# Performance work log

Measured on AMD Instinct MI355X. Metric: run time of the kernel, lower is better.

Reference implementation:

```python
import jax, jax.numpy as jnp
import numpy as np

B, D = 4096, 1024
TEMPERATURE = 0.07


def setup_inputs() -> dict:
    key = jax.random.key(0)
    k1, k2, k3, k4, k5, k6 = jax.random.split(key, 6)
    return {
        "mri_features": jax.random.normal(k1, (B, D), dtype=jnp.float32),
        "pet_features": jax.random.normal(k2, (B, D), dtype=jnp.float32),
        "labels": jax.random.randint(k3, (B,), 0, 3, dtype=jnp.int64),
        "subtype_mri": jax.random.randint(k4, (B,), 0, 4, dtype=jnp.int64),
        "subtype_pet": jax.random.randint(k5, (B,), 0, 4, dtype=jnp.int64),
        "clinical_similarity": jax.random.uniform(k6, (B, B), dtype=jnp.float32),
    }


def _build_weights(labels, subtype_mri, subtype_pet, clinical_similarity):
    # vectorized form of the O(B^2) python loop
    same_label = labels[:, None] == labels[None, :]
    label_zero = labels[:, None] == 0
    sub_match = (subtype_mri[:, None] == subtype_mri[None, :]) & (
        subtype_pet[:, None] == subtype_pet[None, :]
    )
    n = labels.shape[0]
    not_diag = ~jnp.eye(n, dtype=bool)
    mask = same_label & (label_zero | sub_match) & not_diag
    weights = jnp.where(mask, clinical_similarity, 0.0)
    row_sums = weights.sum(axis=1, keepdims=True)
    row_sums = jnp.where(row_sums == 0, 1.0, row_sums)
    return weights / row_sums


def _contrastive(fi, fj, weights):
    fi = fi / jnp.linalg.norm(fi, axis=1, keepdims=True)
    fj = fj / jnp.linalg.norm(fj, axis=1, keepdims=True)
    sim = jnp.matmul(fi, fj.T) / TEMPERATURE  # [B, B]
    log_sm = jax.nn.log_softmax(sim, axis=1)
    return -jnp.sum(weights * log_sm) / fi.shape[0]


def reference(mri_features, pet_features, labels, subtype_mri, subtype_pet, clinical_similarity):
    weights = _build_weights(labels, subtype_mri, subtype_pet, clinical_similarity)
    pairs = [
        (mri_features, pet_features),
        (pet_features, mri_features),
        (mri_features, mri_features),
        (pet_features, pet_features),
    ]
    total = 0.0
    for fi, fj in pairs:
        total = total + _contrastive(fi, fj, weights)
    return total / len(pairs)
```

## Files before the change

### kernel.cpp

```cpp
#include <hip/hip_runtime.h>
#include <hip/hip_bf16.h>
#include <hip/hip_fp8.h>
#include <math.h>

typedef __attribute__((ext_vector_type(4))) float f32x4;

#define NB 4096
#define ND 1024
#define INV_T 14.2857142857142857f

__device__ inline float fp82f(unsigned char b) {
    __hip_fp8_e4m3 h; h.__x = b;
    return (float)h;
}
__device__ inline void gload16(const void* g, void* l) {
    __builtin_amdgcn_global_load_lds(
        (const __attribute__((address_space(1))) void*)g,
        (__attribute__((address_space(3))) void*)l, 16, 0, 0);
}

__global__ __launch_bounds__(256) void norm_kernel(
        const float* __restrict__ M, const float* __restrict__ P,
        unsigned char* __restrict__ Mf, unsigned char* __restrict__ Pf) {
    int row = blockIdx.x & (NB - 1);
    const float* src = (blockIdx.x < NB) ? M : P;
    unsigned char* dst = (blockIdx.x < NB) ? Mf : Pf;
    int tid = threadIdx.x;
    float4 v = ((const float4*)(src + (size_t)row * ND))[tid];
    float ss = v.x * v.x + v.y * v.y + v.z * v.z + v.w * v.w;
    for (int off = 32; off; off >>= 1) ss += __shfl_down(ss, off);
    __shared__ float red[4];
    int lane = tid & 63, w = tid >> 6;
    if (lane == 0) red[w] = ss;
    __syncthreads();
    float rn = rsqrtf(red[0] + red[1] + red[2] + red[3]);
    int p = __builtin_amdgcn_cvt_pk_fp8_f32(v.x * rn, v.y * rn, 0, false);
    p = __builtin_amdgcn_cvt_pk_fp8_f32(v.z * rn, v.w * rn, p, true);
    ((int*)dst)[row * 256 + tid] = p;
}

__global__ __launch_bounds__(256) void key_kernel(
        const int* __restrict__ labels, const int* __restrict__ sm,
        const int* __restrict__ sp, int* __restrict__ code) {
    int i = blockIdx.x * 256 + threadIdx.x;
    if (i < NB) {
        int l = labels[i];
        code[i] = (l == 0) ? 0x40000000 : (1 + l + (sm[i] << 8) + (sp[i] << 16));
    }
}

__global__ __launch_bounds__(256) void rowsumw_kernel(
        const float* __restrict__ cs, const int* __restrict__ code,
        unsigned char* __restrict__ W, float* __restrict__ flag) {
    int i = blockIdx.x;
    int ci = code[i];
    int tid = threadIdx.x;
    const float4* row = (const float4*)(cs + (size_t)i * NB);
    const int4* c4 = (const int4*)code;
    float4 v[4];
    int4 cj[4];
    float s = 0.f;
#pragma unroll
    for (int k = 0; k < 4; ++k) {
        int t = tid + k * 256;
        v[k] = row[t];
        cj[k] = c4[t];
        int j = t * 4;
        if (cj[k].x == ci && j + 0 != i) s += v[k].x;
        if (cj[k].y == ci && j + 1 != i) s += v[k].y;
        if (cj[k].z == ci && j + 2 != i) s += v[k].z;
        if (cj[k].w == ci && j + 3 != i) s += v[k].w;
    }
    for (int off = 1; off < 64; off <<= 1) s += __shfl_xor(s, off);
    __shared__ float red[4];
    int lane = tid & 63, w = tid >> 6;
    if (lane == 0) red[w] = s;
    __syncthreads();
    float tot = red[0] + red[1] + red[2] + red[3];
    float inv = (tot > 0.f) ? 1.f / tot : 0.f;
#pragma unroll
    for (int k = 0; k < 4; ++k) {
        int t = tid + k * 256;
        int j = t * 4;
        float f0 = (cj[k].x == ci && j + 0 != i) ? v[k].x * inv : 0.f;
        float f1 = (cj[k].y == ci && j + 1 != i) ? v[k].y * inv : 0.f;
        float f2 = (cj[k].z == ci && j + 2 != i) ? v[k].z * inv : 0.f;
        float f3 = (cj[k].w == ci && j + 3 != i) ? v[k].w * inv : 0.f;
        int p = __builtin_amdgcn_cvt_pk_fp8_f32(f0, f1, 0, false);
        p = __builtin_amdgcn_cvt_pk_fp8_f32(f2, f3, p, true);
        ((int*)W)[((size_t)i * NB + j) >> 2] = p;
    }
    if (tid == 0) flag[i] = (tot > 0.f) ? 1.f : 0.f;
}

__global__ __launch_bounds__(256, 3) void mega_gemm(
        const unsigned char* __restrict__ Mf, const unsigned char* __restrict__ Pf,
        const unsigned char* __restrict__ Wg,
        float* __restrict__ outs) {
    __shared__ char smem[49152] __attribute__((aligned(16)));

    int tid = threadIdx.x;
    int lane = tid & 63, w = tid >> 6;
    int wm = w >> 1, wn = w & 1;
    int lr = lane & 15, lg = lane >> 4;

    int b = (blockIdx.x & 7) * 260 + (blockIdx.x >> 3);
    int bi, bj, mode;
    const unsigned char *A, *Bm;
    if (b < 1024) {
        int st = b >> 4;
        int sb = b & 15;
        bi = (st >> 3) * 4 + (sb >> 2);
        bj = (st & 7) * 4 + (sb & 3);
        A = Mf; Bm = Pf; mode = 0;
    } else {
        int s = b - 1024;
        int md = (s >= 528) ? 1 : 0;
        s -= md * 528;
        bi = 0;
        while (s >= 32 - bi) { s -= 32 - bi; ++bi; }
        bj = bi + s;
        A = md ? Pf : Mf; Bm = A;
        mode = 1 + md;
    }
    bool offdiag = (bi != bj);
    size_t rowBase = (size_t)bi * 128;
    size_t colBase = (size_t)bj * 128;
    bool needW2 = (rowBase != colBase);
    float* rowTgt = outs + ((mode == 0) ? 0 : (mode == 1) ? 8192 : 12288);
    float* colTgt = (mode == 0) ? (outs + 4096) : rowTgt;

    int sr = lane >> 2;
    int scs = (lane & 3) ^ (sr & 3) ^ ((sr >> 2) & 3);
    const unsigned char* gA = A + (rowBase + w * 32 + sr) * ND + scs * 16;
    const unsigned char* gB = Bm + (colBase + w * 32 + sr) * ND + scs * 16;

    f32x4 acc[4][4] = {};

#define STAGE(bufi, t) {                                                    \
        int k0_ = (t) * 64;                                                 \
        char* baseA_ = smem + (bufi) * 16384;                               \
        char* baseB_ = baseA_ + 8192;                                       \
        gload16(gA + k0_,                   baseA_ + (w * 2    ) * 1024);   \
        gload16(gA + (size_t)16 * ND + k0_, baseA_ + (w * 2 + 1) * 1024);   \
        gload16(gB + k0_,                   baseB_ + (w * 2    ) * 1024);   \
        gload16(gB + (size_t)16 * ND + k0_, baseB_ + (w * 2 + 1) * 1024);   \
    }
#define STAGEW(dst, rbase, cbase) {                                         \
        _Pragma("unroll")                                                   \
        for (int c = 0; c < 4; ++c) {                                       \
            int q_ = w * 4 + c;                                             \
            int sw_ = 8 * q_ + (lane >> 3);                                 \
            int gch_ = (lane & 7) ^ (sw_ & 7);                              \
            gload16(Wg + ((rbase) + sw_) * (size_t)NB + (cbase) + gch_ * 16,\
                    (dst) + q_ * 1024);                                     \
        }                                                                   \
    }
#define COMPUTE(bufi) {                                                     \
        const unsigned char* sA = (const unsigned char*)(smem + (bufi) * 16384); \
        const unsigned char* sB = sA + 8192;                                \
        int rx = (lr & 3) ^ ((lr >> 2) & 3);                                \
        _Pragma("unroll 1")                                                 \
        for (int ks = 0; ks < 2; ++ks) {                                    \
            int cp = (((ks * 2) + (lg >> 1)) ^ rx) * 16 + (lg & 1) * 8;     \
            long av[4], bv[4];                                              \
            _Pragma("unroll")                                               \
            for (int n = 0; n < 4; ++n)                                     \
                bv[n] = *(const long*)&sB[(wn * 64 + n * 16 + lr) * 64 + cp]; \
            _Pragma("unroll")                                               \
            for (int i = 0; i < 4; ++i)                                     \
                av[i] = *(const long*)&sA[(wm * 64 + i * 16 + lr) * 64 + cp]; \
            _Pragma("unroll")                                               \
            for (int i = 0; i < 4; ++i)                                     \
                _Pragma("unroll")                                           \
                for (int n = 0; n < 4; ++n)                                 \
                    acc[i][n] = __builtin_amdgcn_mfma_f32_16x16x32_fp8_fp8( \
                        av[i], bv[n], acc[i][n], 0, 0, 0);                  \
        }                                                                   \
    }
#define BAR __builtin_amdgcn_s_barrier()

    STAGE(0, 0); STAGE(1, 1);
    asm volatile("s_waitcnt vmcnt(4)" ::: "memory"); BAR;
    for (int t = 0; t < 14; ++t) {
        STAGE((t + 2) % 3, t + 2);
        COMPUTE(t % 3);
        asm volatile("s_waitcnt vmcnt(4)" ::: "memory"); BAR;
    }
    STAGEW(smem + 16384, rowBase, colBase);
    COMPUTE(2);
    BAR;
    if (needW2) STAGEW(smem + 32768, colBase, rowBase);
    asm volatile("s_waitcnt vmcnt(0)" ::: "memory"); BAR;
    COMPUTE(0);
#undef STAGE
#undef STAGEW
#undef COMPUTE
#undef BAR

    const unsigned char* wl1 = (const unsigned char*)smem + 16384;
    const unsigned char* wl2 = needW2 ? (const unsigned char*)smem + 32768 : wl1;
    float d1 = 0.f;
    float cexp[4] = {0.f, 0.f, 0.f, 0.f};

#pragma unroll
    for (int m = 0; m < 4; ++m) {
        float rexp[4] = {0.f, 0.f, 0.f, 0.f};
#pragma unroll
        for (int n = 0; n < 4; ++n) {
            int jl = wn * 64 + n * 16 + lr;
#pragma unroll
            for (int r = 0; r < 4; ++r) {
                int rl = wm * 64 + m * 16 + lg * 4 + r;
                float sim = acc[m][n][r] * INV_T;
                float e = __expf(sim - INV_T);
                rexp[r] += e;
                cexp[n] += e;
                float w1v = fp82f(wl1[rl * 128 + (((jl >> 4) ^ (rl & 7)) << 4) + (jl & 15)]);
                float w2v = fp82f(wl2[jl * 128 + (((rl >> 4) ^ (jl & 7)) << 4) + (rl & 15)]);
                d1 += (w1v + w2v) * sim;
            }
        }
#pragma unroll
        for (int r = 0; r < 4; ++r) {
            float v = rexp[r];
            v += __shfl_xor(v, 1); v += __shfl_xor(v, 2);
            v += __shfl_xor(v, 4); v += __shfl_xor(v, 8);
            if (lr == 0)
                atomicAdd(&rowTgt[rowBase + wm * 64 + m * 16 + lg * 4 + r], v);
        }
    }

    if (mode == 0 || offdiag) {
#pragma unroll
        for (int n = 0; n < 4; ++n) {
            float v = cexp[n];
            v += __shfl_xor(v, 16); v += __shfl_xor(v, 32);
            if (lg == 0)
                atomicAdd(&colTgt[colBase + wn * 64 + n * 16 + lr], v);
        }
    }

    float dtot = (mode != 0 && !offdiag) ? 0.5f * d1 : d1;
    for (int off = 32; off; off >>= 1) dtot += __shfl_xor(dtot, off);
    if (lane == 0) {
        float* dots = outs + 16384;
        if (mode == 0) atomicAdd(&dots[0], dtot);
        else           atomicAdd(&dots[1 + mode], dtot);
    }
}

__global__ __launch_bounds__(256) void finalize_kernel(
        const float* __restrict__ outs, const float* __restrict__ flag,
        float* __restrict__ out) {
    const float* rowsum1 = outs;
    const float* colsum1 = outs + 4096;
    const float* rowsum3 = outs + 8192;
    const float* rowsum4 = outs + 12288;
    const float* dots = outs + 16384;
    int tid = threadIdx.x;
    float l = 0.f;
    for (int i = tid; i < NB; i += 256) {
        if (flag[i] != 0.f) {
            l += 4.f * INV_T + logf(rowsum1[i]) + logf(colsum1[i]) +
                 logf(rowsum3[i]) + logf(rowsum4[i]);
        }
    }
    for (int off = 32; off; off >>= 1) l += __shfl_down(l, off);
    __shared__ float red[4];
    int lane = tid & 63, w = tid >> 6;
    if (lane == 0) red[w] = l;
    __syncthreads();
    if (tid == 0) {
        float L = red[0] + red[1] + red[2] + red[3];
        float dt = dots[0] + dots[1] + dots[2] + dots[3];
        out[0] = (L - dt) / (4.0f * (float)NB);
    }
}

extern "C" void kernel_launch(void* const* d_in, const int* in_sizes, int n_in,
                              void* d_out, int out_size, void* d_ws, size_t ws_size,
                              hipStream_t stream) {
    const float* M = (const float*)d_in[0];
    const float* P = (const float*)d_in[1];
    const int* labels = (const int*)d_in[2];
    const int* sm = (const int*)d_in[3];
    const int* sp = (const int*)d_in[4];
    const float* cs = (const float*)d_in[5];
    float* out = (float*)d_out;

    char* ws = (char*)d_ws;
    unsigned char* Mf = (unsigned char*)ws;
    unsigned char* Pf = (unsigned char*)(ws + (size_t)4 * 1024 * 1024);
    unsigned char* W = (unsigned char*)(ws + (size_t)16 * 1024 * 1024);
    char* p = ws + (size_t)48 * 1024 * 1024;
    int* code = (int*)p;    p += 16384;
    float* flag = (float*)p; p += 16384;
    float* outs = (float*)p;

    hipMemsetAsync(outs, 0, 4 * 16384 + 256, stream);

    norm_kernel<<<2 * NB, 256, 0, stream>>>(M, P, Mf, Pf);
    key_kernel<<<NB / 256, 256, 0, stream>>>(labels, sm, sp, code);
    rowsumw_kernel<<<NB, 256, 0, stream>>>(cs, code, W, flag);

    mega_gemm<<<2080, 256, 0, stream>>>(Mf, Pf, W, outs);

    finalize_kernel<<<1, 256, 0, stream>>>(outs, flag, out);
}
```

Baseline: 194.2 us.

## Shrink GEMM tiles to 64x64 single-wave blocks with double buffering

```diff
diff --git a/kernel.cpp b/kernel.cpp
--- a/kernel.cpp
+++ b/kernel.cpp
@@ -93,83 +93,78 @@
     if (tid == 0) flag[i] = (tot > 0.f) ? 1.f : 0.f;
 }
 
-__global__ __launch_bounds__(256, 3) void mega_gemm(
+__global__ __launch_bounds__(64) void mega_gemm(
         const unsigned char* __restrict__ Mf, const unsigned char* __restrict__ Pf,
         const unsigned char* __restrict__ Wg,
         float* __restrict__ outs) {
-    __shared__ char smem[49152] __attribute__((aligned(16)));
-
-    int tid = threadIdx.x;
-    int lane = tid & 63, w = tid >> 6;
-    int wm = w >> 1, wn = w & 1;
+    __shared__ char smem[16384] __attribute__((aligned(16)));
+
+    int lane = threadIdx.x;
     int lr = lane & 15, lg = lane >> 4;
 
-    int b = (blockIdx.x & 7) * 260 + (blockIdx.x >> 3);
+    int b = (blockIdx.x & 7) * 1032 + (blockIdx.x >> 3);
     int bi, bj, mode;
     const unsigned char *A, *Bm;
-    if (b < 1024) {
+    if (b < 4096) {
         int st = b >> 4;
         int sb = b & 15;
-        bi = (st >> 3) * 4 + (sb >> 2);
-        bj = (st & 7) * 4 + (sb & 3);
+        bi = (st >> 4) * 4 + (sb >> 2);
+        bj = (st & 15) * 4 + (sb & 3);
         A = Mf; Bm = Pf; mode = 0;
     } else {
-        int s = b - 1024;
-        int md = (s >= 528) ? 1 : 0;
-        s -= md * 528;
+        int s = b - 4096;
+        int md = (s >= 2080) ? 1 : 0;
+        s -= md * 2080;
         bi = 0;
-        while (s >= 32 - bi) { s -= 32 - bi; ++bi; }
+        while (s >= 64 - bi) { s -= 64 - bi; ++bi; }
         bj = bi + s;
         A = md ? Pf : Mf; Bm = A;
         mode = 1 + md;
     }
     bool offdiag = (bi != bj);
-    size_t rowBase = (size_t)bi * 128;
-    size_t colBase = (size_t)bj * 128;
+    size_t rowBase = (size_t)bi * 64;
+    size_t colBase = (size_t)bj * 64;
     bool needW2 = (rowBase != colBase);
     float* rowTgt = outs + ((mode == 0) ? 0 : (mode == 1) ? 8192 : 12288);
     float* colTgt = (mode == 0) ? (outs + 4096) : rowTgt;
 
     int sr = lane >> 2;
     int scs = (lane & 3) ^ (sr & 3) ^ ((sr >> 2) & 3);
-    const unsigned char* gA = A + (rowBase + w * 32 + sr) * ND + scs * 16;
-    const unsigned char* gB = Bm + (colBase + w * 32 + sr) * ND + scs * 16;
+    const unsigned char* gA = A + (rowBase + sr) * ND + scs * 16;
+    const unsigned char* gB = Bm + (colBase + sr) * ND + scs * 16;
 
     f32x4 acc[4][4] = {};
 
 #define STAGE(bufi, t) {                                                    \
         int k0_ = (t) * 64;                                                 \
-        char* baseA_ = smem + (bufi) * 16384;                               \
-        char* baseB_ = baseA_ + 8192;                                       \
-        gload16(gA + k0_,                   baseA_ + (w * 2    ) * 1024);   \
-        gload16(gA + (size_t)16 * ND + k0_, baseA_ + (w * 2 + 1) * 1024);   \
-        gload16(gB + k0_,                   baseB_ + (w * 2    ) * 1024);   \
-        gload16(gB + (size_t)16 * ND + k0_, baseB_ + (w * 2 + 1) * 1024);   \
+        char* base_ = smem + (bufi) * 8192;                                 \
+        _Pragma("unroll")                                                   \
+        for (int c = 0; c < 4; ++c) {                                       \
+            gload16(gA + (size_t)(c * 16) * ND + k0_, base_ + c * 1024);    \
+            gload16(gB + (size_t)(c * 16) * ND + k0_, base_ + 4096 + c * 1024); \
+        }                                                                   \
     }
 #define STAGEW(dst, rbase, cbase) {                                         \
         _Pragma("unroll")                                                   \
         for (int c = 0; c < 4; ++c) {                                       \
-            int q_ = w * 4 + c;                                             \
-            int sw_ = 8 * q_ + (lane >> 3);                                 \
-            int gch_ = (lane & 7) ^ (sw_ & 7);                              \
-            gload16(Wg + ((rbase) + sw_) * (size_t)NB + (cbase) + gch_ * 16,\
-                    (dst) + q_ * 1024);                                     \
+            gload16(Wg + ((rbase) + c * 16 + sr) * (size_t)NB + (cbase) + scs * 16, \
+                    (dst) + c * 1024);                                      \
         }                                                                   \
     }
 #define COMPUTE(bufi) {                                                     \
-        const unsigned char* sA = (const unsigned char*)(smem + (bufi) * 16384); \
-        const unsigned char* sB = sA + 8192;                                \
+        const unsigned char* sA = (const unsigned char*)(smem + (bufi) * 8192); \
+        const unsigned char* sB = sA + 4096;                                \
         int rx = (lr & 3) ^ ((lr >> 2) & 3);                                \
-        _Pragma("unroll 1")                                                 \
+        _Pragma("unroll")                                                   \
         for (int ks = 0; ks < 2; ++ks) {                                    \
             int cp = (((ks * 2) + (lg >> 1)) ^ rx) * 16 + (lg & 1) * 8;     \
             long av[4], bv[4];                                              \
             _Pragma("unroll")                                               \
             for (int n = 0; n < 4; ++n)                                     \
-                bv[n] = *(const long*)&sB[(wn * 64 + n * 16 + lr) * 64 + cp]; \
+                bv[n] = *(const long*)&sB[(n * 16 + lr) * 64 + cp];         \
             _Pragma("unroll")                                               \
             for (int i = 0; i < 4; ++i)                                     \
-                av[i] = *(const long*)&sA[(wm * 64 + i * 16 + lr) * 64 + cp]; \
+                av[i] = *(const long*)&sA[(i * 16 + lr) * 64 + cp];         \
             _Pragma("unroll")                                               \
             for (int i = 0; i < 4; ++i)                                     \
                 _Pragma("unroll")                                           \
@@ -177,29 +172,31 @@
                     acc[i][n] = __builtin_amdgcn_mfma_f32_16x16x32_fp8_fp8( \
                         av[i], bv[n], acc[i][n], 0, 0, 0);                  \
         }                                                                   \
-    }
-#define BAR __builtin_amdgcn_s_barrier()
-
-    STAGE(0, 0); STAGE(1, 1);
-    asm volatile("s_waitcnt vmcnt(4)" ::: "memory"); BAR;
-    for (int t = 0; t < 14; ++t) {
-        STAGE((t + 2) % 3, t + 2);
-        COMPUTE(t % 3);
-        asm volatile("s_waitcnt vmcnt(4)" ::: "memory"); BAR;
-    }
-    STAGEW(smem + 16384, rowBase, colBase);
-    COMPUTE(2);
-    BAR;
-    if (needW2) STAGEW(smem + 32768, colBase, rowBase);
-    asm volatile("s_waitcnt vmcnt(0)" ::: "memory"); BAR;
-    COMPUTE(0);
+        asm volatile("s_waitcnt lgkmcnt(0)" ::: "memory");                  \
+    }
+
+    STAGE(0, 0);
+    for (int t = 0; t < 15; ++t) {
+        STAGE((t + 1) & 1, t + 1);
+        asm volatile("s_waitcnt vmcnt(8)" ::: "memory");
+        COMPUTE(t & 1);
+    }
+    STAGEW(smem, rowBase, colBase);
+    if (needW2) {
+        STAGEW(smem + 4096, colBase, rowBase);
+        asm volatile("s_waitcnt vmcnt(8)" ::: "memory");
+    } else {
+        asm volatile("s_waitcnt vmcnt(4)" ::: "memory");
+    }
+    COMPUTE(1);
+    asm volatile("s_waitcnt vmcnt(0)" ::: "memory");
 #undef STAGE
 #undef STAGEW
 #undef COMPUTE
-#undef BAR
-
-    const unsigned char* wl1 = (const unsigned char*)smem + 16384;
-    const unsigned char* wl2 = needW2 ? (const unsigned char*)smem + 32768 : wl1;
+
+    const unsigned char* wl1 = (const unsigned char*)smem;
+    const unsigned char* wl2 = needW2 ? (const unsigned char*)smem + 4096
+                                      : (const unsigned char*)smem;
     float d1 = 0.f;
     float cexp[4] = {0.f, 0.f, 0.f, 0.f};
 
@@ -208,16 +205,18 @@
         float rexp[4] = {0.f, 0.f, 0.f, 0.f};
 #pragma unroll
         for (int n = 0; n < 4; ++n) {
-            int jl = wn * 64 + n * 16 + lr;
+            int jl = n * 16 + lr;
 #pragma unroll
             for (int r = 0; r < 4; ++r) {
-                int rl = wm * 64 + m * 16 + lg * 4 + r;
+                int rl = m * 16 + lg * 4 + r;
                 float sim = acc[m][n][r] * INV_T;
                 float e = __expf(sim - INV_T);
                 rexp[r] += e;
                 cexp[n] += e;
-                float w1v = fp82f(wl1[rl * 128 + (((jl >> 4) ^ (rl & 7)) << 4) + (jl & 15)]);
-                float w2v = fp82f(wl2[jl * 128 + (((rl >> 4) ^ (jl & 7)) << 4) + (rl & 15)]);
+                float w1v = fp82f(wl1[rl * 64 +
+                    (((jl >> 4) ^ (rl & 3) ^ ((rl >> 2) & 3)) << 4) + (jl & 15)]);
+                float w2v = fp82f(wl2[jl * 64 +
+                    (((rl >> 4) ^ (jl & 3) ^ ((jl >> 2) & 3)) << 4) + (rl & 15)]);
                 d1 += (w1v + w2v) * sim;
             }
         }
@@ -227,7 +226,7 @@
             v += __shfl_xor(v, 1); v += __shfl_xor(v, 2);
             v += __shfl_xor(v, 4); v += __shfl_xor(v, 8);
             if (lr == 0)
-                atomicAdd(&rowTgt[rowBase + wm * 64 + m * 16 + lg * 4 + r], v);
+                atomicAdd(&rowTgt[rowBase + m * 16 + lg * 4 + r], v);
         }
     }
 
@@ -237,7 +236,7 @@
             float v = cexp[n];
             v += __shfl_xor(v, 16); v += __shfl_xor(v, 32);
             if (lg == 0)
-                atomicAdd(&colTgt[colBase + wn * 64 + n * 16 + lr], v);
+                atomicAdd(&colTgt[colBase + n * 16 + lr], v);
         }
     }
 
@@ -304,7 +303,7 @@
     key_kernel<<<NB / 256, 256, 0, stream>>>(labels, sm, sp, code);
     rowsumw_kernel<<<NB, 256, 0, stream>>>(cs, code, W, flag);
 
-    mega_gemm<<<2080, 256, 0, stream>>>(Mf, Pf, W, outs);
+    mega_gemm<<<8256, 64, 0, stream>>>(Mf, Pf, W, outs);
 
     finalize_kernel<<<1, 256, 0, stream>>>(outs, flag, out);
 }
```

Result: faster. 188.3 us (-3.0%).

## Use 256x256 GEMM tiles and pre-symmetrize weight matrix in separate kernel

Applied to the files above, without the earlier changes.

```diff
diff --git a/kernel.cpp b/kernel.cpp
--- a/kernel.cpp
+++ b/kernel.cpp
@@ -93,40 +93,70 @@
     if (tid == 0) flag[i] = (tot > 0.f) ? 1.f : 0.f;
 }
 
-__global__ __launch_bounds__(256, 3) void mega_gemm(
+__global__ __launch_bounds__(256) void symw_kernel(unsigned char* __restrict__ W) {
+    __shared__ unsigned char Ta[64][80], Tb[64][80];
+    int b = blockIdx.x;
+    int ti = 0, t = b;
+    while (t >= 64 - ti) { t -= 64 - ti; ++ti; }
+    int tj = ti + t;
+    size_t ra = (size_t)ti * 64, rb = (size_t)tj * 64;
+    int tid = threadIdx.x;
+    int r = tid >> 2, c0 = (tid & 3) * 16;
+    int4 a0 = *(const int4*)&W[(ra + r) * NB + rb + c0];
+    int4 b0 = *(const int4*)&W[(rb + r) * NB + ra + c0];
+    *(int4*)&Ta[r][c0] = a0;
+    *(int4*)&Tb[r][c0] = b0;
+    __syncthreads();
+    unsigned char oa[16], ob[16];
+#pragma unroll
+    for (int c = 0; c < 16; c += 2) {
+        int cc = c0 + c;
+        float a_lo = fp82f(Ta[r][cc])     + fp82f(Tb[cc][r]);
+        float a_hi = fp82f(Ta[r][cc + 1]) + fp82f(Tb[cc + 1][r]);
+        float b_lo = fp82f(Tb[r][cc])     + fp82f(Ta[cc][r]);
+        float b_hi = fp82f(Tb[r][cc + 1]) + fp82f(Ta[cc + 1][r]);
+        int pa = __builtin_amdgcn_cvt_pk_fp8_f32(a_lo, a_hi, 0, false);
+        int pb = __builtin_amdgcn_cvt_pk_fp8_f32(b_lo, b_hi, 0, false);
+        oa[c] = (unsigned char)(pa & 0xff); oa[c + 1] = (unsigned char)((pa >> 8) & 0xff);
+        ob[c] = (unsigned char)(pb & 0xff); ob[c + 1] = (unsigned char)((pb >> 8) & 0xff);
+    }
+    *(int4*)&W[(ra + r) * NB + rb + c0] = *(int4*)&oa[0];
+    *(int4*)&W[(rb + r) * NB + ra + c0] = *(int4*)&ob[0];
+}
+
+__global__ __launch_bounds__(512) void mega_gemm(
         const unsigned char* __restrict__ Mf, const unsigned char* __restrict__ Pf,
         const unsigned char* __restrict__ Wg,
         float* __restrict__ outs) {
-    __shared__ char smem[49152] __attribute__((aligned(16)));
+    __shared__ char smem[98304] __attribute__((aligned(16)));
 
     int tid = threadIdx.x;
     int lane = tid & 63, w = tid >> 6;
-    int wm = w >> 1, wn = w & 1;
+    int wm = w >> 2, wn = w & 3;
     int lr = lane & 15, lg = lane >> 4;
 
-    int b = (blockIdx.x & 7) * 260 + (blockIdx.x >> 3);
+    int b = (blockIdx.x & 7) * 66 + (blockIdx.x >> 3);
     int bi, bj, mode;
     const unsigned char *A, *Bm;
-    if (b < 1024) {
-        int st = b >> 4;
-        int sb = b & 15;
-        bi = (st >> 3) * 4 + (sb >> 2);
-        bj = (st & 7) * 4 + (sb & 3);
+    if (b < 256) {
+        int st = b >> 2;
+        int sb = b & 3;
+        bi = (st >> 3) * 2 + (sb >> 1);
+        bj = (st & 7) * 2 + (sb & 1);
         A = Mf; Bm = Pf; mode = 0;
     } else {
-        int s = b - 1024;
-        int md = (s >= 528) ? 1 : 0;
-        s -= md * 528;
+        int s = b - 256;
+        int md = (s >= 136) ? 1 : 0;
+        s -= md * 136;
         bi = 0;
-        while (s >= 32 - bi) { s -= 32 - bi; ++bi; }
+        while (s >= 16 - bi) { s -= 16 - bi; ++bi; }
         bj = bi + s;
         A = md ? Pf : Mf; Bm = A;
         mode = 1 + md;
     }
     bool offdiag = (bi != bj);
-    size_t rowBase = (size_t)bi * 128;
-    size_t colBase = (size_t)bj * 128;
-    bool needW2 = (rowBase != colBase);
+    size_t rowBase = (size_t)bi * 256;
+    size_t colBase = (size_t)bj * 256;
     float* rowTgt = outs + ((mode == 0) ? 0 : (mode == 1) ? 8192 : 12288);
     float* colTgt = (mode == 0) ? (outs + 4096) : rowTgt;
 
@@ -135,47 +165,51 @@
     const unsigned char* gA = A + (rowBase + w * 32 + sr) * ND + scs * 16;
     const unsigned char* gB = Bm + (colBase + w * 32 + sr) * ND + scs * 16;
 
-    f32x4 acc[4][4] = {};
+    f32x4 acc[8][4] = {};
 
 #define STAGE(bufi, t) {                                                    \
         int k0_ = (t) * 64;                                                 \
-        char* baseA_ = smem + (bufi) * 16384;                               \
-        char* baseB_ = baseA_ + 8192;                                       \
+        char* baseA_ = smem + (bufi) * 32768;                               \
+        char* baseB_ = baseA_ + 16384;                                      \
         gload16(gA + k0_,                   baseA_ + (w * 2    ) * 1024);   \
         gload16(gA + (size_t)16 * ND + k0_, baseA_ + (w * 2 + 1) * 1024);   \
         gload16(gB + k0_,                   baseB_ + (w * 2    ) * 1024);   \
         gload16(gB + (size_t)16 * ND + k0_, baseB_ + (w * 2 + 1) * 1024);   \
     }
-#define STAGEW(dst, rbase, cbase) {                                         \
+#define STAGEW(dst, rbase) {                                                \
         _Pragma("unroll")                                                   \
         for (int c = 0; c < 4; ++c) {                                       \
-            int q_ = w * 4 + c;                                             \
-            int sw_ = 8 * q_ + (lane >> 3);                                 \
-            int gch_ = (lane & 7) ^ (sw_ & 7);                              \
-            gload16(Wg + ((rbase) + sw_) * (size_t)NB + (cbase) + gch_ * 16,\
+            int q_ = w * 4 + c;                                  \
+            int swl_ = 4 * q_ + (lane >> 4);          \
+            int gch_ = (lane & 15) ^ (swl_ & 7);       \
+            gload16(Wg + ((rbase) + swl_) * (size_t)NB + colBase + gch_ * 16,\
                     (dst) + q_ * 1024);                                     \
         }                                                                   \
     }
 #define COMPUTE(bufi) {                                                     \
-        const unsigned char* sA = (const unsigned char*)(smem + (bufi) * 16384); \
-        const unsigned char* sB = sA + 8192;                                \
+        const unsigned char* sA = (const unsigned char*)(smem + (bufi) * 32768); \
+        const unsigned char* sB = sA + 16384;                               \
         int rx = (lr & 3) ^ ((lr >> 2) & 3);                                \
-        _Pragma("unroll 1")                                                 \
+        _Pragma("unroll")                                                   \
         for (int ks = 0; ks < 2; ++ks) {                                    \
             int cp = (((ks * 2) + (lg >> 1)) ^ rx) * 16 + (lg & 1) * 8;     \
-            long av[4], bv[4];                                              \
+            long bv[4];                                                     \
             _Pragma("unroll")                                               \
             for (int n = 0; n < 4; ++n)                                     \
                 bv[n] = *(const long*)&sB[(wn * 64 + n * 16 + lr) * 64 + cp]; \
             _Pragma("unroll")                                               \
-            for (int i = 0; i < 4; ++i)                                     \
-                av[i] = *(const long*)&sA[(wm * 64 + i * 16 + lr) * 64 + cp]; \
-            _Pragma("unroll")                                               \
-            for (int i = 0; i < 4; ++i)                                     \
+            for (int mh = 0; mh < 2; ++mh) {                                \
+                long av[4];                                                 \
                 _Pragma("unroll")                                           \
-                for (int n = 0; n < 4; ++n)                                 \
-                    acc[i][n] = __builtin_amdgcn_mfma_f32_16x16x32_fp8_fp8( \
-                        av[i], bv[n], acc[i][n], 0, 0, 0);                  \
+                for (int i = 0; i < 4; ++i)                                 \
+                    av[i] = *(const long*)&sA[(wm * 128 + (mh * 4 + i) * 16 + lr) * 64 + cp]; \
+                _Pragma("unroll")                                           \
+                for (int i = 0; i < 4; ++i)                                 \
+                    _Pragma("unroll")                                       \
+                    for (int n = 0; n < 4; ++n)                             \
+                        acc[mh * 4 + i][n] = __builtin_amdgcn_mfma_f32_16x16x32_fp8_fp8( \
+                            av[i], bv[n], acc[mh * 4 + i][n], 0, 0, 0);     \
+            }                                                               \
         }                                                                   \
     }
 #define BAR __builtin_amdgcn_s_barrier()
@@ -187,38 +221,37 @@
         COMPUTE(t % 3);
         asm volatile("s_waitcnt vmcnt(4)" ::: "memory"); BAR;
     }
-    STAGEW(smem + 16384, rowBase, colBase);
+    STAGEW(smem + 32768, rowBase);
     COMPUTE(2);
     BAR;
-    if (needW2) STAGEW(smem + 32768, colBase, rowBase);
+    STAGEW(smem + 65536, rowBase + 128);
+    asm volatile("s_waitcnt vmcnt(8)" ::: "memory"); BAR;
+    COMPUTE(0);
     asm volatile("s_waitcnt vmcnt(0)" ::: "memory"); BAR;
-    COMPUTE(0);
 #undef STAGE
 #undef STAGEW
 #undef COMPUTE
 #undef BAR
 
-    const unsigned char* wl1 = (const unsigned char*)smem + 16384;
-    const unsigned char* wl2 = needW2 ? (const unsigned char*)smem + 32768 : wl1;
+    const unsigned char* wl = (const unsigned char*)smem + 32768 + wm * 32768;
     float d1 = 0.f;
     float cexp[4] = {0.f, 0.f, 0.f, 0.f};
 
 #pragma unroll
-    for (int m = 0; m < 4; ++m) {
+    for (int m = 0; m < 8; ++m) {
         float rexp[4] = {0.f, 0.f, 0.f, 0.f};
 #pragma unroll
         for (int n = 0; n < 4; ++n) {
             int jl = wn * 64 + n * 16 + lr;
 #pragma unroll
             for (int r = 0; r < 4; ++r) {
-                int rl = wm * 64 + m * 16 + lg * 4 + r;
+                int rl = m * 16 + lg * 4 + r;
                 float sim = acc[m][n][r] * INV_T;
                 float e = __expf(sim - INV_T);
                 rexp[r] += e;
                 cexp[n] += e;
-                float w1v = fp82f(wl1[rl * 128 + (((jl >> 4) ^ (rl & 7)) << 4) + (jl & 15)]);
-                float w2v = fp82f(wl2[jl * 128 + (((rl >> 4) ^ (jl & 7)) << 4) + (rl & 15)]);
-                d1 += (w1v + w2v) * sim;
+                int ck = (jl >> 4) ^ (rl & 7);
+                d1 += fp82f(wl[rl * 256 + ck * 16 + (jl & 15)]) * sim;
             }
         }
 #pragma unroll
@@ -227,7 +260,7 @@
             v += __shfl_xor(v, 1); v += __shfl_xor(v, 2);
             v += __shfl_xor(v, 4); v += __shfl_xor(v, 8);
             if (lr == 0)
-                atomicAdd(&rowTgt[rowBase + wm * 64 + m * 16 + lg * 4 + r], v);
+                atomicAdd(&rowTgt[rowBase + wm * 128 + m * 16 + lg * 4 + r], v);
         }
     }
 
@@ -303,8 +336,9 @@
     norm_kernel<<<2 * NB, 256, 0, stream>>>(M, P, Mf, Pf);
     key_kernel<<<NB / 256, 256, 0, stream>>>(labels, sm, sp, code);
     rowsumw_kernel<<<NB, 256, 0, stream>>>(cs, code, W, flag);
-
-    mega_gemm<<<2080, 256, 0, stream>>>(Mf, Pf, W, outs);
+    symw_kernel<<<2080, 256, 0, stream>>>(W);
+
+    mega_gemm<<<528, 512, 0, stream>>>(Mf, Pf, W, outs);
 
     finalize_kernel<<<1, 256, 0, stream>>>(outs, flag, out);
 }
```

Result: slower. 235.7 us (+21.4%).
